# Kernel optimization log

Measured on AMD Instinct MI355X. Metric: run time of the kernel, lower is better.

Reference implementation:

```python
import jax, jax.numpy as jnp
import numpy as np

NSITES = 100000
NYEARS = 20
NVIS = 2
HDIM = 64


def setup_inputs() -> dict:
    key = jax.random.key(0)
    ks = jax.random.split(key, 10)
    def w(k, shape, fan_in):
        return (jax.random.normal(k, shape, jnp.float32) / np.sqrt(fan_in)).astype(jnp.float32)
    return {
        "sxy0": jax.random.normal(ks[0], (1, NSITES, 1), jnp.float32),
        "sxy": jax.random.normal(ks[1], (NSITES, NYEARS - 1, 1), jnp.float32),
        "oxy": jax.random.normal(ks[2], (NSITES, NYEARS, NVIS), jnp.float32),
        # to_h0: Linear(1 -> 64)
        "W_h0": w(ks[3], (HDIM, 1), 1), "b_h0": jnp.zeros((HDIM,), jnp.float32),
        # to_h1: Linear(64 -> 64)
        "W_h1": w(ks[4], (HDIM, HDIM), HDIM), "b_h1": jnp.zeros((HDIM,), jnp.float32),
        # to_hrnn: RNN(input=1, hidden=64, relu)
        "W_ih": w(ks[5], (HDIM, 1), 1), "b_ih": jnp.zeros((HDIM,), jnp.float32),
        "W_hh": w(ks[6], (HDIM, HDIM), HDIM), "b_hh": jnp.zeros((HDIM,), jnp.float32),
        # to_psi0 / to_psi: Linear(64 -> 1)
        "W_psi0": w(ks[7], (1, HDIM), HDIM), "b_psi0": jnp.zeros((1,), jnp.float32),
        "W_psi": w(ks[8], (1, HDIM), HDIM), "b_psi": jnp.zeros((1,), jnp.float32),
        # to_p: Linear(65 -> 1)
        "W_p": w(ks[9], (1, HDIM + 1), HDIM + 1), "b_p": jnp.zeros((1,), jnp.float32),
    }


def reference(sxy0, sxy, oxy, W_h0, b_h0, W_h1, b_h1, W_ih, b_ih, W_hh, b_hh,
              W_psi0, b_psi0, W_psi, b_psi, W_p, b_p):
    # site embeddings -> initial hidden state
    hs = jax.nn.elu(sxy0 @ W_h0.T + b_h0)            # [1, N, H]
    h0 = jax.nn.elu(hs @ W_h1.T + b_h1)              # [1, N, H]

    # single-layer relu RNN, batch_first: sxy [N, T, 1], h0 [1, N, H]
    xs = jnp.swapaxes(sxy, 0, 1)                     # [T, N, 1]
    def step(h, x):
        h_new = jax.nn.relu(x @ W_ih.T + b_ih + h @ W_hh.T + b_hh)
        return h_new, h_new
    _, h_seq = jax.lax.scan(step, h0[0], xs)         # [T, N, H]
    h_out = jnp.swapaxes(h_seq, 0, 1)                # [N, T, H]

    psi0_out = jax.nn.sigmoid(h0 @ W_psi0.T + b_psi0)   # [1, N, 1]
    psi_out = jax.nn.sigmoid(h_out @ W_psi.T + b_psi)   # [N, T, 1]

    # detection prob p[i, t, j] = sigmoid(to_p(cat(H[i, t], oxy[i, t, j])))
    # where H[:, 0] = h0 and H[:, t] = h_out[:, t-1] for t >= 1
    H = jnp.concatenate([h0[0][:, None, :], h_out], axis=1)  # [N, Y, H]
    logits = H @ W_p[:, :HDIM].T + oxy * W_p[0, HDIM] + b_p  # [N, Y, NVIS]
    p = jax.nn.sigmoid(logits)
    return psi0_out, psi_out, p
```

## Files before the change

kernel.cpp:

```cpp
#include <hip/hip_runtime.h>
#include <math.h>

#define NSITES 100000
#define NYEARS 20
#define HDIM 64
#define WSTR 72

typedef _Float16 f16x8 __attribute__((ext_vector_type(8)));
typedef _Float16 hx2   __attribute__((ext_vector_type(2)));
typedef float f32x4 __attribute__((ext_vector_type(4)));

__device__ __forceinline__ float sigmoidf_(float x) { return 1.0f / (1.0f + __expf(-x)); }
__device__ __forceinline__ float eluf_(float x) { return x > 0.0f ? x : __expf(x) - 1.0f; }

__device__ __forceinline__ unsigned pack2h_(float a, float b) {
    union { _Float16 h; unsigned short u; } x, y;
    x.h = (_Float16)a; y.h = (_Float16)b;
    return ((unsigned)y.u << 16) | (unsigned)x.u;
}

__device__ __forceinline__ f16x8 cvt8h_(const float* p) {
    float4 a = ((const float4*)p)[0];
    float4 b = ((const float4*)p)[1];
    f16x8 r;
    r[0] = (_Float16)a.x; r[1] = (_Float16)a.y; r[2] = (_Float16)a.z; r[3] = (_Float16)a.w;
    r[4] = (_Float16)b.x; r[5] = (_Float16)b.y; r[6] = (_Float16)b.z; r[7] = (_Float16)b.w;
    return r;
}

__device__ __forceinline__ f16x8 ldsfrag_(const unsigned short* b, int row, int off) {
    union { f16x8 v; uint4 u; } r;
    r.u = *(const uint4*)&b[row * WSTR + off];
    return r.v;
}

union FragU { hx2 h2[4]; f16x8 v; };

__global__ __launch_bounds__(256, 2)
void rnet_kernel(const float* __restrict__ sxy0,
                 const float* __restrict__ sxy,
                 const float* __restrict__ oxy,
                 const float* __restrict__ W_h0, const float* __restrict__ b_h0,
                 const float* __restrict__ W_h1, const float* __restrict__ b_h1,
                 const float* __restrict__ W_ih, const float* __restrict__ b_ih,
                 const float* __restrict__ W_hh, const float* __restrict__ b_hh,
                 const float* __restrict__ W_psi0, const float* __restrict__ b_psi0,
                 const float* __restrict__ W_psi, const float* __restrict__ b_psi,
                 const float* __restrict__ W_p, const float* __restrict__ b_p,
                 float* __restrict__ out)
{
    const int tid  = threadIdx.x;
    const int lane = tid & 63;
    const int wv   = tid >> 6;
    const int s = lane & 15;
    const int q = lane >> 4;
    const int sq = s >> 2, sr = s & 3;
    const int base = blockIdx.x * 64;
    const int sl   = wv * 16 + s;
    const int site = base + sl;
    const int site_ld = site < NSITES ? site : NSITES - 1;

    __shared__ __align__(16) unsigned short wbuf[2 * 64 * WSTR];
    unsigned short* const whh_l = wbuf;
    unsigned short* const wh1_l = wbuf + 64 * WSTR;
    float* const pL   = (float*)wbuf;
    float* const psiL = (float*)wbuf + 64 * 20;

    float* __restrict__ out_psi0 = out;
    float* __restrict__ out_psi  = out + NSITES;
    float* __restrict__ out_p    = out + 20 * NSITES;

    {
        const float4* whg = (const float4*)W_hh;
        const float4* w1g = (const float4*)W_h1;
#pragma unroll
        for (int j = 0; j < 4; ++j) {
            int e4 = j * 256 + tid;
            int row = e4 >> 4, c4 = e4 & 15;
            float4 a = whg[e4];
            uint2 pa; pa.x = pack2h_(a.x, a.y); pa.y = pack2h_(a.z, a.w);
            *(uint2*)&whh_l[row * WSTR + c4 * 4] = pa;
            float4 b = w1g[e4];
            uint2 pb; pb.x = pack2h_(b.x, b.y); pb.y = pack2h_(b.z, b.w);
            *(uint2*)&wh1_l[row * WSTR + c4 * 4] = pb;
        }
    }
    __syncthreads();

    f16x8 bf[2];
    {
        const float s0v = sxy0[site_ld];
        f16x8 bf0[2];
#pragma unroll
        for (int kt = 0; kt < 2; ++kt) {
            const float* wp = W_h0 + kt * 32 + q * 8;
            const float* bp = b_h0 + kt * 32 + q * 8;
            float4 w0 = ((const float4*)wp)[0], w1 = ((const float4*)wp)[1];
            float4 c0 = ((const float4*)bp)[0], c1 = ((const float4*)bp)[1];
            float v[8];
            v[0] = eluf_(fmaf(s0v, w0.x, c0.x)); v[1] = eluf_(fmaf(s0v, w0.y, c0.y));
            v[2] = eluf_(fmaf(s0v, w0.z, c0.z)); v[3] = eluf_(fmaf(s0v, w0.w, c0.w));
            v[4] = eluf_(fmaf(s0v, w1.x, c1.x)); v[5] = eluf_(fmaf(s0v, w1.y, c1.y));
            v[6] = eluf_(fmaf(s0v, w1.z, c1.z)); v[7] = eluf_(fmaf(s0v, w1.w, c1.w));
#pragma unroll
            for (int j = 0; j < 8; ++j) bf0[kt][j] = (_Float16)v[j];
        }

        f32x4 acc[4];
#pragma unroll
        for (int mt = 0; mt < 4; ++mt) {
            const int dr = 32 * (mt >> 1) + 8 * q + 4 * (mt & 1);
            float4 b1 = *(const float4*)(b_h1 + dr);
            acc[mt][0] = b1.x; acc[mt][1] = b1.y; acc[mt][2] = b1.z; acc[mt][3] = b1.w;
        }
#pragma unroll
        for (int kt = 0; kt < 2; ++kt)
#pragma unroll
            for (int mt = 0; mt < 4; ++mt) {
                const int ar = 32 * (mt >> 1) + 8 * sq + 4 * (mt & 1) + sr;
                f16x8 a = ldsfrag_(wh1_l, ar, kt * 32 + q * 8);
                acc[mt] = __builtin_amdgcn_mfma_f32_16x16x32_f16(a, bf0[kt], acc[mt], 0, 0, 0);
            }
        FragU f0, f1;
#pragma unroll
        for (int mt = 0; mt < 4; ++mt) {
            hx2 plo; plo[0] = (_Float16)eluf_(acc[mt][0]); plo[1] = (_Float16)eluf_(acc[mt][1]);
            hx2 phi; phi[0] = (_Float16)eluf_(acc[mt][2]); phi[1] = (_Float16)eluf_(acc[mt][3]);
            if (mt < 2) { f0.h2[mt * 2] = plo; f0.h2[mt * 2 + 1] = phi; }
            else        { f1.h2[(mt - 2) * 2] = plo; f1.h2[(mt - 2) * 2 + 1] = phi; }
        }
        bf[0] = f0.v;
        bf[1] = f1.v;
    }

    f16x8 a_hh[4][2];
#pragma unroll
    for (int mt = 0; mt < 4; ++mt) {
        const int ar = 32 * (mt >> 1) + 8 * sq + 4 * (mt & 1) + sr;
#pragma unroll
        for (int kt = 0; kt < 2; ++kt)
            a_hh[mt][kt] = ldsfrag_(whh_l, ar, kt * 32 + q * 8);
    }

    __syncthreads();

    f16x8 a_head[2];
    {
        const float* hrow = (s == 1) ? W_p : ((s == 2) ? W_psi0 : W_psi);
#pragma unroll
        for (int kt = 0; kt < 2; ++kt) a_head[kt] = cvt8h_(hrow + kt * 32 + q * 8);
    }
    f32x4 biasD[4];
    hx2 wih2[4][2];
#pragma unroll
    for (int mt = 0; mt < 4; ++mt) {
        const int dr = 32 * (mt >> 1) + 8 * q + 4 * (mt & 1);
        float4 bi = *(const float4*)(b_ih + dr);
        float4 bh = *(const float4*)(b_hh + dr);
        float4 wi = *(const float4*)(W_ih + dr);
        biasD[mt][0] = bi.x + bh.x; biasD[mt][1] = bi.y + bh.y;
        biasD[mt][2] = bi.z + bh.z; biasD[mt][3] = bi.w + bh.w;
        wih2[mt][0][0] = (_Float16)wi.x; wih2[mt][0][1] = (_Float16)wi.y;
        wih2[mt][1][0] = (_Float16)wi.z; wih2[mt][1][1] = (_Float16)wi.w;
    }
    f32x4 headC;
    headC[0] = (q == 0) ? b_psi[0]  : 0.0f;
    headC[1] = (q == 0) ? b_p[0]    : 0.0f;
    headC[2] = (q == 0) ? b_psi0[0] : 0.0f;
    headC[3] = 0.0f;
    const hx2 z2 = (hx2)(_Float16)0.0f;
    const float* __restrict__ xs_g = sxy + (size_t)site_ld * 19;

    float x = xs_g[0];
#pragma unroll 1
    for (int t = 1; t < NYEARS; ++t) {
        float x_next = (t < NYEARS - 1) ? xs_g[t] : 0.0f;

        f32x4 acc[4], accH;
#pragma unroll
        for (int mt = 0; mt < 4; ++mt)
            acc[mt] = __builtin_amdgcn_mfma_f32_16x16x32_f16(a_hh[mt][0], bf[0], biasD[mt], 0, 0, 0);
        accH = __builtin_amdgcn_mfma_f32_16x16x32_f16(a_head[0], bf[0], headC, 0, 0, 0);
#pragma unroll
        for (int mt = 0; mt < 4; ++mt)
            acc[mt] = __builtin_amdgcn_mfma_f32_16x16x32_f16(a_hh[mt][1], bf[1], acc[mt], 0, 0, 0);
        accH = __builtin_amdgcn_mfma_f32_16x16x32_f16(a_head[1], bf[1], accH, 0, 0, 0);

        _Float16 xh = (_Float16)x;
        hx2 x2; x2[0] = xh; x2[1] = xh;
        FragU f0, f1;
#pragma unroll
        for (int mt = 0; mt < 4; ++mt) {
            hx2 plo; plo[0] = (_Float16)acc[mt][0]; plo[1] = (_Float16)acc[mt][1];
            hx2 phi; phi[0] = (_Float16)acc[mt][2]; phi[1] = (_Float16)acc[mt][3];
            plo = __builtin_elementwise_max(plo + x2 * wih2[mt][0], z2);
            phi = __builtin_elementwise_max(phi + x2 * wih2[mt][1], z2);
            if (mt < 2) { f0.h2[mt * 2] = plo; f0.h2[mt * 2 + 1] = phi; }
            else        { f1.h2[(mt - 2) * 2] = plo; f1.h2[(mt - 2) * 2 + 1] = phi; }
        }
        bf[0] = f0.v;
        bf[1] = f1.v;

        if (q == 0) {
            pL[sl * 20 + (t - 1)]   = accH[1];
            psiL[sl * 20 + (t - 1)] = accH[0];
            if (t == 1) psiL[sl * 20] = accH[2];
        }
        x = x_next;
    }

    {
        f32x4 accH = __builtin_amdgcn_mfma_f32_16x16x32_f16(a_head[0], bf[0], headC, 0, 0, 0);
        accH = __builtin_amdgcn_mfma_f32_16x16x32_f16(a_head[1], bf[1], accH, 0, 0, 0);
        if (q == 0) {
            pL[sl * 20 + 19]   = accH[1];
            psiL[sl * 20 + 19] = accH[0];
        }
    }

    __syncthreads();

    const float wpo = W_p[HDIM];
    if (tid < 64 && base + tid < NSITES) out_psi0[base + tid] = sigmoidf_(psiL[tid * 20]);
#pragma unroll
    for (int r = 0; r < 5; ++r) {
        int i = r * 256 + tid;
        if (i < 64 * 19 && (size_t)base * 19 + i < (size_t)NSITES * 19) {
            int s2 = i / 19, c = i - s2 * 19;
            out_psi[(size_t)base * 19 + i] = sigmoidf_(psiL[s2 * 20 + c + 1]);
        }
    }
    const float4* oxy_b = (const float4*)(oxy + (size_t)base * 40);
    float4* outp_b = (float4*)(out_p + (size_t)base * 40);
    const int p4max = (NSITES * 40) / 4;
#pragma unroll
    for (int r = 0; r < 3; ++r) {
        int i4 = r * 256 + tid;
        if (i4 < 640 && blockIdx.x * 640 + i4 < p4max) {
            float4 ox = oxy_b[i4];
            float lg0 = pL[i4 * 2];
            float lg1 = pL[i4 * 2 + 1];
            float4 pv;
            pv.x = sigmoidf_(fmaf(wpo, ox.x, lg0));
            pv.y = sigmoidf_(fmaf(wpo, ox.y, lg0));
            pv.z = sigmoidf_(fmaf(wpo, ox.z, lg1));
            pv.w = sigmoidf_(fmaf(wpo, ox.w, lg1));
            outp_b[i4] = pv;
        }
    }
}

extern "C" void kernel_launch(void* const* d_in, const int* in_sizes, int n_in,
                              void* d_out, int out_size, void* d_ws, size_t ws_size,
                              hipStream_t stream) {
    const float* sxy0   = (const float*)d_in[0];
    const float* sxy    = (const float*)d_in[1];
    const float* oxy    = (const float*)d_in[2];
    const float* W_h0   = (const float*)d_in[3];
    const float* b_h0   = (const float*)d_in[4];
    const float* W_h1   = (const float*)d_in[5];
    const float* b_h1   = (const float*)d_in[6];
    const float* W_ih   = (const float*)d_in[7];
    const float* b_ih   = (const float*)d_in[8];
    const float* W_hh   = (const float*)d_in[9];
    const float* b_hh   = (const float*)d_in[10];
    const float* W_psi0 = (const float*)d_in[11];
    const float* b_psi0 = (const float*)d_in[12];
    const float* W_psi  = (const float*)d_in[13];
    const float* b_psi  = (const float*)d_in[14];
    const float* W_p    = (const float*)d_in[15];
    const float* b_p    = (const float*)d_in[16];

    float* out = (float*)d_out;

    dim3 block(256);
    dim3 grid((NSITES + 63) / 64);
    rnet_kernel<<<grid, block, 0, stream>>>(
        sxy0, sxy, oxy, W_h0, b_h0, W_h1, b_h1, W_ih, b_ih, W_hh, b_hh,
        W_psi0, b_psi0, W_psi, b_psi, W_p, b_p, out);
}
```

Measured before the change: 136.0 us.

## Use single-wave blocks loading weights directly from global memory

Shrinks each block from four waves covering 64 sites to one wave covering 16 sites, and drops the shared-memory staging of W_hh and W_h1. Each lane now converts its MFMA weight fragments straight from global memory, which removes the staging copy and the block-wide barriers. In exchange, four times as many blocks each re-read the weights from global memory or cache. The tail bounds checks are removed on the assumption that NSITES is a multiple of 16.

```diff
diff --git a/kernel.cpp b/kernel.cpp
--- a/kernel.cpp
+++ b/kernel.cpp
@@ -4,7 +4,6 @@
 #define NSITES 100000
 #define NYEARS 20
 #define HDIM 64
-#define WSTR 72
 
 typedef _Float16 f16x8 __attribute__((ext_vector_type(8)));
 typedef _Float16 hx2   __attribute__((ext_vector_type(2)));
@@ -12,12 +11,6 @@
 
 __device__ __forceinline__ float sigmoidf_(float x) { return 1.0f / (1.0f + __expf(-x)); }
 __device__ __forceinline__ float eluf_(float x) { return x > 0.0f ? x : __expf(x) - 1.0f; }
-
-__device__ __forceinline__ unsigned pack2h_(float a, float b) {
-    union { _Float16 h; unsigned short u; } x, y;
-    x.h = (_Float16)a; y.h = (_Float16)b;
-    return ((unsigned)y.u << 16) | (unsigned)x.u;
-}
 
 __device__ __forceinline__ f16x8 cvt8h_(const float* p) {
     float4 a = ((const float4*)p)[0];
@@ -28,15 +21,9 @@
     return r;
 }
 
-__device__ __forceinline__ f16x8 ldsfrag_(const unsigned short* b, int row, int off) {
-    union { f16x8 v; uint4 u; } r;
-    r.u = *(const uint4*)&b[row * WSTR + off];
-    return r.v;
-}
-
 union FragU { hx2 h2[4]; f16x8 v; };
 
-__global__ __launch_bounds__(256, 2)
+__global__ __launch_bounds__(64, 4)
 void rnet_kernel(const float* __restrict__ sxy0,
                  const float* __restrict__ sxy,
                  const float* __restrict__ oxy,
@@ -49,47 +36,23 @@
                  const float* __restrict__ W_p, const float* __restrict__ b_p,
                  float* __restrict__ out)
 {
-    const int tid  = threadIdx.x;
-    const int lane = tid & 63;
-    const int wv   = tid >> 6;
+    const int lane = threadIdx.x;
     const int s = lane & 15;
     const int q = lane >> 4;
     const int sq = s >> 2, sr = s & 3;
-    const int base = blockIdx.x * 64;
-    const int sl   = wv * 16 + s;
-    const int site = base + sl;
-    const int site_ld = site < NSITES ? site : NSITES - 1;
-
-    __shared__ __align__(16) unsigned short wbuf[2 * 64 * WSTR];
-    unsigned short* const whh_l = wbuf;
-    unsigned short* const wh1_l = wbuf + 64 * WSTR;
-    float* const pL   = (float*)wbuf;
-    float* const psiL = (float*)wbuf + 64 * 20;
+    const int base = blockIdx.x * 16;
+    const int site = base + s;
+
+    __shared__ __align__(16) float pL[16 * 20];
+    __shared__ __align__(16) float psiL[16 * 20];
 
     float* __restrict__ out_psi0 = out;
     float* __restrict__ out_psi  = out + NSITES;
     float* __restrict__ out_p    = out + 20 * NSITES;
 
-    {
-        const float4* whg = (const float4*)W_hh;
-        const float4* w1g = (const float4*)W_h1;
-#pragma unroll
-        for (int j = 0; j < 4; ++j) {
-            int e4 = j * 256 + tid;
-            int row = e4 >> 4, c4 = e4 & 15;
-            float4 a = whg[e4];
-            uint2 pa; pa.x = pack2h_(a.x, a.y); pa.y = pack2h_(a.z, a.w);
-            *(uint2*)&whh_l[row * WSTR + c4 * 4] = pa;
-            float4 b = w1g[e4];
-            uint2 pb; pb.x = pack2h_(b.x, b.y); pb.y = pack2h_(b.z, b.w);
-            *(uint2*)&wh1_l[row * WSTR + c4 * 4] = pb;
-        }
-    }
-    __syncthreads();
-
     f16x8 bf[2];
     {
-        const float s0v = sxy0[site_ld];
+        const float s0v = sxy0[site];
         f16x8 bf0[2];
 #pragma unroll
         for (int kt = 0; kt < 2; ++kt) {
@@ -118,7 +81,7 @@
 #pragma unroll
             for (int mt = 0; mt < 4; ++mt) {
                 const int ar = 32 * (mt >> 1) + 8 * sq + 4 * (mt & 1) + sr;
-                f16x8 a = ldsfrag_(wh1_l, ar, kt * 32 + q * 8);
+                f16x8 a = cvt8h_(W_h1 + ar * HDIM + kt * 32 + q * 8);
                 acc[mt] = __builtin_amdgcn_mfma_f32_16x16x32_f16(a, bf0[kt], acc[mt], 0, 0, 0);
             }
         FragU f0, f1;
@@ -139,11 +102,8 @@
         const int ar = 32 * (mt >> 1) + 8 * sq + 4 * (mt & 1) + sr;
 #pragma unroll
         for (int kt = 0; kt < 2; ++kt)
-            a_hh[mt][kt] = ldsfrag_(whh_l, ar, kt * 32 + q * 8);
-    }
-
-    __syncthreads();
-
+            a_hh[mt][kt] = cvt8h_(W_hh + ar * HDIM + kt * 32 + q * 8);
+    }
     f16x8 a_head[2];
     {
         const float* hrow = (s == 1) ? W_p : ((s == 2) ? W_psi0 : W_psi);
@@ -169,7 +129,7 @@
     headC[2] = (q == 0) ? b_psi0[0] : 0.0f;
     headC[3] = 0.0f;
     const hx2 z2 = (hx2)(_Float16)0.0f;
-    const float* __restrict__ xs_g = sxy + (size_t)site_ld * 19;
+    const float* __restrict__ xs_g = sxy + (size_t)site * 19;
 
     float x = xs_g[0];
 #pragma unroll 1
@@ -202,9 +162,9 @@
         bf[1] = f1.v;
 
         if (q == 0) {
-            pL[sl * 20 + (t - 1)]   = accH[1];
-            psiL[sl * 20 + (t - 1)] = accH[0];
-            if (t == 1) psiL[sl * 20] = accH[2];
+            pL[s * 20 + (t - 1)]   = accH[1];
+            psiL[s * 20 + (t - 1)] = accH[0];
+            if (t == 1) psiL[s * 20] = accH[2];
         }
         x = x_next;
     }
@@ -213,30 +173,29 @@
         f32x4 accH = __builtin_amdgcn_mfma_f32_16x16x32_f16(a_head[0], bf[0], headC, 0, 0, 0);
         accH = __builtin_amdgcn_mfma_f32_16x16x32_f16(a_head[1], bf[1], accH, 0, 0, 0);
         if (q == 0) {
-            pL[sl * 20 + 19]   = accH[1];
-            psiL[sl * 20 + 19] = accH[0];
+            pL[s * 20 + 19]   = accH[1];
+            psiL[s * 20 + 19] = accH[0];
         }
     }
 
     __syncthreads();
 
     const float wpo = W_p[HDIM];
-    if (tid < 64 && base + tid < NSITES) out_psi0[base + tid] = sigmoidf_(psiL[tid * 20]);
+    if (lane < 16) out_psi0[base + lane] = sigmoidf_(psiL[lane * 20]);
 #pragma unroll
     for (int r = 0; r < 5; ++r) {
-        int i = r * 256 + tid;
-        if (i < 64 * 19 && (size_t)base * 19 + i < (size_t)NSITES * 19) {
+        int i = r * 64 + lane;
+        if (i < 16 * 19) {
             int s2 = i / 19, c = i - s2 * 19;
             out_psi[(size_t)base * 19 + i] = sigmoidf_(psiL[s2 * 20 + c + 1]);
         }
     }
     const float4* oxy_b = (const float4*)(oxy + (size_t)base * 40);
     float4* outp_b = (float4*)(out_p + (size_t)base * 40);
-    const int p4max = (NSITES * 40) / 4;
 #pragma unroll
     for (int r = 0; r < 3; ++r) {
-        int i4 = r * 256 + tid;
-        if (i4 < 640 && blockIdx.x * 640 + i4 < p4max) {
+        int i4 = r * 64 + lane;
+        if (i4 < 160) {
             float4 ox = oxy_b[i4];
             float lg0 = pL[i4 * 2];
             float lg1 = pL[i4 * 2 + 1];
@@ -273,8 +232,8 @@
 
     float* out = (float*)d_out;
 
-    dim3 block(256);
-    dim3 grid((NSITES + 63) / 64);
+    dim3 block(64);
+    dim3 grid(NSITES / 16);
     rnet_kernel<<<grid, block, 0, stream>>>(
         sxy0, sxy, oxy, W_h0, b_h0, W_h1, b_h1, W_ih, b_ih, W_hh, b_hh,
         W_psi0, b_psi0, W_psi, b_psi, W_p, b_p, out);
```

Result: slower. 169.9 us (+25.0%).

## Stream RNN weight fragments from LDS each step to raise occupancy

Applied to the files above, without the earlier changes.

W_hh fragments and head weights are no longer held in registers across the recurrence. Each step reloads them from LDS, using fixed base offsets that an empty asm keeps from being hoisted. The W_h1 LDS copy is dropped in favour of direct global loads, and the recurrent bias is now added in fp16 after the MFMA instead of seeding the accumulator. Launch bounds rise from 2 to 8 waves per SIMD to hide the latency of the serial recurrence. The cost is extra LDS traffic every step and slightly lower bias precision.

```diff
diff --git a/kernel.cpp b/kernel.cpp
--- a/kernel.cpp
+++ b/kernel.cpp
@@ -13,10 +13,11 @@
 __device__ __forceinline__ float sigmoidf_(float x) { return 1.0f / (1.0f + __expf(-x)); }
 __device__ __forceinline__ float eluf_(float x) { return x > 0.0f ? x : __expf(x) - 1.0f; }
 
+__device__ __forceinline__ unsigned short h16_(float a) {
+    union { _Float16 h; unsigned short u; } x; x.h = (_Float16)a; return x.u;
+}
 __device__ __forceinline__ unsigned pack2h_(float a, float b) {
-    union { _Float16 h; unsigned short u; } x, y;
-    x.h = (_Float16)a; y.h = (_Float16)b;
-    return ((unsigned)y.u << 16) | (unsigned)x.u;
+    return ((unsigned)h16_(b) << 16) | (unsigned)h16_(a);
 }
 
 __device__ __forceinline__ f16x8 cvt8h_(const float* p) {
@@ -28,15 +29,15 @@
     return r;
 }
 
-__device__ __forceinline__ f16x8 ldsfrag_(const unsigned short* b, int row, int off) {
+__device__ __forceinline__ f16x8 ldsb_(const char* base, unsigned boff, int imm) {
     union { f16x8 v; uint4 u; } r;
-    r.u = *(const uint4*)&b[row * WSTR + off];
+    r.u = *(const uint4*)(base + boff + imm);
     return r.v;
 }
 
 union FragU { hx2 h2[4]; f16x8 v; };
 
-__global__ __launch_bounds__(256, 2)
+__global__ __launch_bounds__(256, 8)
 void rnet_kernel(const float* __restrict__ sxy0,
                  const float* __restrict__ sxy,
                  const float* __restrict__ oxy,
@@ -60,11 +61,9 @@
     const int site = base + sl;
     const int site_ld = site < NSITES ? site : NSITES - 1;
 
-    __shared__ __align__(16) unsigned short wbuf[2 * 64 * WSTR];
-    unsigned short* const whh_l = wbuf;
-    unsigned short* const wh1_l = wbuf + 64 * WSTR;
-    float* const pL   = (float*)wbuf;
-    float* const psiL = (float*)wbuf + 64 * 20;
+    __shared__ __align__(16) unsigned short whh_l[68 * WSTR];
+    __shared__ __align__(16) float pL[64 * 20];
+    __shared__ __align__(16) float psiL[64 * 20];
 
     float* __restrict__ out_psi0 = out;
     float* __restrict__ out_psi  = out + NSITES;
@@ -72,7 +71,6 @@
 
     {
         const float4* whg = (const float4*)W_hh;
-        const float4* w1g = (const float4*)W_h1;
 #pragma unroll
         for (int j = 0; j < 4; ++j) {
             int e4 = j * 256 + tid;
@@ -80,9 +78,11 @@
             float4 a = whg[e4];
             uint2 pa; pa.x = pack2h_(a.x, a.y); pa.y = pack2h_(a.z, a.w);
             *(uint2*)&whh_l[row * WSTR + c4 * 4] = pa;
-            float4 b = w1g[e4];
-            uint2 pb; pb.x = pack2h_(b.x, b.y); pb.y = pack2h_(b.z, b.w);
-            *(uint2*)&wh1_l[row * WSTR + c4 * 4] = pb;
+        }
+        if (tid < 192) {
+            int r = tid >> 6, c = tid & 63;
+            const float* src = (r == 0) ? W_psi : ((r == 1) ? W_p : W_psi0);
+            whh_l[(64 + r) * WSTR + c] = h16_(src[c]);
         }
     }
     __syncthreads();
@@ -118,7 +118,7 @@
 #pragma unroll
             for (int mt = 0; mt < 4; ++mt) {
                 const int ar = 32 * (mt >> 1) + 8 * sq + 4 * (mt & 1) + sr;
-                f16x8 a = ldsfrag_(wh1_l, ar, kt * 32 + q * 8);
+                f16x8 a = cvt8h_(W_h1 + ar * HDIM + kt * 32 + q * 8);
                 acc[mt] = __builtin_amdgcn_mfma_f32_16x16x32_f16(a, bf0[kt], acc[mt], 0, 0, 0);
             }
         FragU f0, f1;
@@ -133,68 +133,57 @@
         bf[1] = f1.v;
     }
 
-    f16x8 a_hh[4][2];
-#pragma unroll
-    for (int mt = 0; mt < 4; ++mt) {
-        const int ar = 32 * (mt >> 1) + 8 * sq + 4 * (mt & 1) + sr;
-#pragma unroll
-        for (int kt = 0; kt < 2; ++kt)
-            a_hh[mt][kt] = ldsfrag_(whh_l, ar, kt * 32 + q * 8);
-    }
-
-    __syncthreads();
-
-    f16x8 a_head[2];
-    {
-        const float* hrow = (s == 1) ? W_p : ((s == 2) ? W_psi0 : W_psi);
-#pragma unroll
-        for (int kt = 0; kt < 2; ++kt) a_head[kt] = cvt8h_(hrow + kt * 32 + q * 8);
-    }
-    f32x4 biasD[4];
-    hx2 wih2[4][2];
+    const int hsel = (s == 1) ? 1 : ((s == 2) ? 2 : 0);
+    unsigned ahh_off = (unsigned)(((8 * sq + sr) * WSTR + q * 8) * 2);
+    unsigned ahd_off = (unsigned)(((64 + hsel) * WSTR + q * 8) * 2);
+    hx2 wih2[4][2], bias2[4][2];
 #pragma unroll
     for (int mt = 0; mt < 4; ++mt) {
         const int dr = 32 * (mt >> 1) + 8 * q + 4 * (mt & 1);
         float4 bi = *(const float4*)(b_ih + dr);
         float4 bh = *(const float4*)(b_hh + dr);
         float4 wi = *(const float4*)(W_ih + dr);
-        biasD[mt][0] = bi.x + bh.x; biasD[mt][1] = bi.y + bh.y;
-        biasD[mt][2] = bi.z + bh.z; biasD[mt][3] = bi.w + bh.w;
+        bias2[mt][0][0] = (_Float16)(bi.x + bh.x); bias2[mt][0][1] = (_Float16)(bi.y + bh.y);
+        bias2[mt][1][0] = (_Float16)(bi.z + bh.z); bias2[mt][1][1] = (_Float16)(bi.w + bh.w);
         wih2[mt][0][0] = (_Float16)wi.x; wih2[mt][0][1] = (_Float16)wi.y;
         wih2[mt][1][0] = (_Float16)wi.z; wih2[mt][1][1] = (_Float16)wi.w;
     }
-    f32x4 headC;
-    headC[0] = (q == 0) ? b_psi[0]  : 0.0f;
-    headC[1] = (q == 0) ? b_p[0]    : 0.0f;
-    headC[2] = (q == 0) ? b_psi0[0] : 0.0f;
-    headC[3] = 0.0f;
+    const float bpsiS  = b_psi[0];
+    const float bpS    = b_p[0];
+    const float bpsi0S = b_psi0[0];
+    f32x4 zc; zc[0] = 0.0f; zc[1] = 0.0f; zc[2] = 0.0f; zc[3] = 0.0f;
     const hx2 z2 = (hx2)(_Float16)0.0f;
     const float* __restrict__ xs_g = sxy + (size_t)site_ld * 19;
+    const char* wb = (const char*)whh_l;
+#define OFFH(mt, kt) ((32 * ((mt) >> 1) + 4 * ((mt) & 1)) * 144 + (kt) * 64)
 
     float x = xs_g[0];
 #pragma unroll 1
     for (int t = 1; t < NYEARS; ++t) {
         float x_next = (t < NYEARS - 1) ? xs_g[t] : 0.0f;
+        asm volatile("" : "+v"(ahh_off), "+v"(ahd_off));
 
         f32x4 acc[4], accH;
 #pragma unroll
         for (int mt = 0; mt < 4; ++mt)
-            acc[mt] = __builtin_amdgcn_mfma_f32_16x16x32_f16(a_hh[mt][0], bf[0], biasD[mt], 0, 0, 0);
-        accH = __builtin_amdgcn_mfma_f32_16x16x32_f16(a_head[0], bf[0], headC, 0, 0, 0);
+            acc[mt] = __builtin_amdgcn_mfma_f32_16x16x32_f16(ldsb_(wb, ahh_off, OFFH(mt, 0)), bf[0], zc, 0, 0, 0);
+        accH = __builtin_amdgcn_mfma_f32_16x16x32_f16(ldsb_(wb, ahd_off, 0), bf[0], zc, 0, 0, 0);
 #pragma unroll
         for (int mt = 0; mt < 4; ++mt)
-            acc[mt] = __builtin_amdgcn_mfma_f32_16x16x32_f16(a_hh[mt][1], bf[1], acc[mt], 0, 0, 0);
-        accH = __builtin_amdgcn_mfma_f32_16x16x32_f16(a_head[1], bf[1], accH, 0, 0, 0);
+            acc[mt] = __builtin_amdgcn_mfma_f32_16x16x32_f16(ldsb_(wb, ahh_off, OFFH(mt, 1)), bf[1], acc[mt], 0, 0, 0);
+        accH = __builtin_amdgcn_mfma_f32_16x16x32_f16(ldsb_(wb, ahd_off, 64), bf[1], accH, 0, 0, 0);
 
         _Float16 xh = (_Float16)x;
         hx2 x2; x2[0] = xh; x2[1] = xh;
         FragU f0, f1;
 #pragma unroll
         for (int mt = 0; mt < 4; ++mt) {
+            hx2 xlo = x2 * wih2[mt][0] + bias2[mt][0];
+            hx2 xhi = x2 * wih2[mt][1] + bias2[mt][1];
             hx2 plo; plo[0] = (_Float16)acc[mt][0]; plo[1] = (_Float16)acc[mt][1];
             hx2 phi; phi[0] = (_Float16)acc[mt][2]; phi[1] = (_Float16)acc[mt][3];
-            plo = __builtin_elementwise_max(plo + x2 * wih2[mt][0], z2);
-            phi = __builtin_elementwise_max(phi + x2 * wih2[mt][1], z2);
+            plo = __builtin_elementwise_max(plo + xlo, z2);
+            phi = __builtin_elementwise_max(phi + xhi, z2);
             if (mt < 2) { f0.h2[mt * 2] = plo; f0.h2[mt * 2 + 1] = phi; }
             else        { f1.h2[(mt - 2) * 2] = plo; f1.h2[(mt - 2) * 2 + 1] = phi; }
         }
@@ -202,19 +191,19 @@
         bf[1] = f1.v;
 
         if (q == 0) {
-            pL[sl * 20 + (t - 1)]   = accH[1];
-            psiL[sl * 20 + (t - 1)] = accH[0];
-            if (t == 1) psiL[sl * 20] = accH[2];
+            pL[sl * 20 + (t - 1)]   = accH[1] + bpS;
+            psiL[sl * 20 + (t - 1)] = accH[0] + bpsiS;
+            if (t == 1) psiL[sl * 20] = accH[2] + bpsi0S;
         }
         x = x_next;
     }
 
     {
-        f32x4 accH = __builtin_amdgcn_mfma_f32_16x16x32_f16(a_head[0], bf[0], headC, 0, 0, 0);
-        accH = __builtin_amdgcn_mfma_f32_16x16x32_f16(a_head[1], bf[1], accH, 0, 0, 0);
+        f32x4 accH = __builtin_amdgcn_mfma_f32_16x16x32_f16(ldsb_(wb, ahd_off, 0), bf[0], zc, 0, 0, 0);
+        accH = __builtin_amdgcn_mfma_f32_16x16x32_f16(ldsb_(wb, ahd_off, 64), bf[1], accH, 0, 0, 0);
         if (q == 0) {
-            pL[sl * 20 + 19]   = accH[1];
-            psiL[sl * 20 + 19] = accH[0];
+            pL[sl * 20 + 19]   = accH[1] + bpS;
+            psiL[sl * 20 + 19] = accH[0] + bpsiS;
         }
     }
 
@@ -248,6 +237,7 @@
             outp_b[i4] = pv;
         }
     }
+#undef OFFH
 }
 
 extern "C" void kernel_launch(void* const* d_in, const int* in_sizes, int n_in,
```

After: 143.1 us. +5.2%, slower.
